# Optimization experiments

Measured on AMD Instinct MI355X. Metric: run time of the kernel, lower is better.

Reference implementation:

```python
import jax, jax.numpy as jnp
import numpy as np

N, G = 10000, 200          # nodes, graphs
EL, EG = 160000, 500000    # local / global edges
S, V = 256, 64             # scalar / vector hidden dims
NA, NB = 16, 5             # atom types, bond types


def _lin(k, i, o):
    return (jax.random.normal(k, (i, o), jnp.float32) / np.sqrt(i))


def scatter_mean(vals, idx, num_segments):
    # vals: [N, ...]; idx: [N] int
    sums = jax.ops.segment_sum(vals, idx, num_segments=num_segments)
    cnt = jax.ops.segment_sum(jnp.ones((vals.shape[0],), vals.dtype), idx,
                              num_segments=num_segments)
    cnt = jnp.maximum(cnt, 1.0).reshape((-1,) + (1,) * (vals.ndim - 1))
    return sums / cnt


def calc_edge_attrs(edge_index, pos):
    src, tgt = edge_index[0], edge_index[1]
    r = pos[tgt] - pos[src]                      # [E,3]
    a = (pos[tgt] * pos[src]).sum(-1)            # [E]
    d = jnp.sqrt(jnp.clip((r ** 2).sum(-1), 1e-6))
    r_norm = r / d[:, None]
    return d, a, r_norm


def setup_inputs() -> dict:
    key = jax.random.key(0)
    ks = jax.random.split(key, 24)
    inp = {}
    inp["x"] = jax.random.normal(ks[0], (N, NA), jnp.float32)
    inp["t"] = jax.random.uniform(ks[1], (G, 1), jnp.float32)
    inp["pos"] = jax.random.normal(ks[2], (N, 3), jnp.float32)
    eil = jax.random.randint(ks[3], (2, EL), 0, N)
    eig = jax.random.randint(ks[4], (2, EG), 0, N)
    # avoid self-edges so edge distances are strictly positive (safe sqrt grads)
    eig = eig.at[1].set(jnp.where(eig[1] == eig[0], (eig[1] + 1) % N, eig[1]))
    eil = eil.at[1].set(jnp.where(eil[1] == eil[0], (eil[1] + 1) % N, eil[1]))
    inp["edge_index_local"] = eil
    inp["edge_index_global"] = eig
    inp["edge_attr_global"] = jax.random.normal(ks[5], (EG, NB), jnp.float32)
    inp["batch"] = jnp.sort(jax.random.randint(ks[6], (N,), 0, G))
    # learned parameters
    inp["W_time"], inp["b_time"] = _lin(ks[7], 1, S), jnp.zeros((S,), jnp.float32)
    inp["W_atom"], inp["b_atom"] = _lin(ks[8], NA, S), jnp.zeros((S,), jnp.float32)
    inp["W_at"], inp["b_at"] = _lin(ks[9], S, S), jnp.zeros((S,), jnp.float32)
    inp["W_shared"], inp["b_shared"] = _lin(ks[10], S, S), jnp.zeros((S,), jnp.float32)
    inp["W_b0"], inp["b_b0"] = _lin(ks[11], S + 1, S), jnp.zeros((S,), jnp.float32)
    inp["W_b1"], inp["b_b1"] = _lin(ks[12], S, 2 * NB), jnp.zeros((2 * NB,), jnp.float32)
    inp["W_coord"] = _lin(ks[13], V, 2)           # no bias
    inp["W_atoms"], inp["b_atoms"] = _lin(ks[14], S, 2 * NA), jnp.zeros((2 * NA,), jnp.float32)
    return inp


def reference(x, t, pos, edge_attr_global, W_time, b_time, W_atom, b_atom,
              W_at, b_at, W_shared, b_shared, W_b0, b_b0, W_b1, b_b1,
              W_coord, W_atoms, b_atoms,
              edge_index_local, edge_index_global, batch):
    # --- trunk: center positions, embed atoms + time ---
    pos = pos - scatter_mean(pos, batch, G)[batch]
    temb = t @ W_time + b_time                    # [G,S]
    tnode = temb[batch]                           # [N,S]
    s = x @ W_atom + b_atom
    s = (s + tnode) @ W_at + b_at                 # [N,S]
    # --- edge attrs (gather-compute pattern feeding the GNN) ---
    d_l, a_l, rn_l = calc_edge_attrs(edge_index_local, pos)
    d_g, a_g, rn_g = calc_edge_attrs(edge_index_global, pos)
    # GNN stand-in (identity on s, v, p): v initialized to zeros as in original
    v = jnp.zeros((N, 3, V), s.dtype)
    # --- prediction head ---
    s = jax.nn.silu(s @ W_shared + b_shared)
    j, i = edge_index_global[0], edge_index_global[1]
    d = jnp.sqrt(((pos[i] - pos[j]) ** 2).sum(-1, keepdims=True))  # [EG,1]
    edge = jnp.concatenate([s[i] + s[j], d], axis=-1)              # [EG,S+1]
    bonds = jax.nn.silu(edge @ W_b0 + b_b0) @ W_b1 + b_b1          # [EG,2*NB]
    bonds_pred, bonds_eps = bonds[:, :NB], bonds[:, NB:]
    coords = jnp.einsum('nkv,vo->nko', v, W_coord)                 # [N,3,2]
    coords = coords - scatter_mean(coords, batch, G)[batch]
    coords_eps0, coords_eps1 = coords[..., 0], coords[..., 1]      # [N,3]
    atoms = s @ W_atoms + b_atoms                                  # [N,2*NA]
    atoms_eps, atoms_pred = atoms[:, :NA], atoms[:, NA:]
    pos_c = pos - scatter_mean(pos, batch, G)[batch]
    coords_pred = pos_c + coords_eps1
    return (coords_pred, coords_eps0, atoms_pred, atoms_eps,
            bonds_pred, bonds_eps, d_l, rn_l, a_g, rn_g)
```

## Files before the change

kernel.cpp:

```cpp
#include <hip/hip_runtime.h>
#include <hip/hip_bf16.h>

typedef __hip_bfloat16 bf16;
typedef short bf16x8 __attribute__((ext_vector_type(8)));
typedef float f32x4 __attribute__((ext_vector_type(4)));
typedef float f32x2 __attribute__((ext_vector_type(2)));

#define N_NODES  10000
#define G_GRAPHS 200
#define EL_EDGES 160000
#define EG_EDGES 500000
#define S_DIM    256
#define APAD     264

#define WS_FLAG   0
#define WS_POSC   1024
#define WS_WD     31232
#define WS_BB0    31488
#define WS_BB1    34304
#define WS_WATOM  34560
#define WS_WTIME  38656
#define WS_BTIME  38912
#define WS_BATOM  39168
#define WS_BAT    39424
#define WS_BSH    39680
#define WS_BATOMS 39936
#define WS_T      40000
#define WS_X      40448
#define WT_AT     200448
#define WT_SH     233216
#define WT_B0     265984
#define WT_ATOMS  298752
#define WT_B1     302848
#define WS_H      304896
#define WS_END_FLOATS (WS_H + (N_NODES * S_DIM) / 4)

#define CHAN(S)    ((((S) >> 6) << 6) + (((S) & 3) << 4) + (((S) & 63) >> 2))
#define CHANINV(k) ((((k) >> 6) << 6) + (((k) & 15) << 2) + (((k) >> 4) & 3))

#define O_CPRED 0
#define O_CEPS  30000
#define O_APRED 60000
#define O_AEPS  220000
#define O_BPRED 380000
#define O_BEPS  2880000
#define O_DL    5380000
#define O_RNL   5540000
#define O_AG    6020000
#define O_RNG   6520000

__device__ __forceinline__ float b2f(bf16 v) { return __bfloat162float(v); }
__device__ __forceinline__ bf16  f2b(float v) { return __float2bfloat16(v); }
__device__ __forceinline__ unsigned short bbits(float v) {
    bf16 b = f2b(v);
    return *reinterpret_cast<unsigned short*>(&b);
}
__device__ __forceinline__ float ldin(const void* p, int idx, int isf32) {
    return isf32 ? ((const float*)p)[idx] : b2f(((const bf16*)p)[idx]);
}
__device__ __forceinline__ void stout(void* out, int f32o, size_t idx, float v) {
    if (f32o) ((float*)out)[idx] = v;
    else      ((bf16*)out)[idx]  = f2b(v);
}
__device__ __forceinline__ float silu(float p) {
    return p * __builtin_amdgcn_rcpf(1.0f + __expf(-p));
}
__device__ __forceinline__ int dtype_f32(const void* tt) {
    const unsigned short* q = (const unsigned short*)tt;
    int c = 0;
#pragma unroll
    for (int z = 0; z < 32; ++z) c += (q[z] >= 0x4000) ? 1 : 0;
    return c > 0;
}

__global__ void k_prep(const void* __restrict__ x, const void* __restrict__ tt,
                       const void* __restrict__ W_time, const void* __restrict__ b_time,
                       const void* __restrict__ W_atom, const void* __restrict__ b_atom,
                       const void* __restrict__ W_at, const void* __restrict__ b_at,
                       const void* __restrict__ W_shared, const void* __restrict__ b_shared,
                       const void* __restrict__ W_b0, const void* __restrict__ b_b0,
                       const void* __restrict__ W_b1, const void* __restrict__ b_b1,
                       const void* __restrict__ W_atoms, const void* __restrict__ b_atoms,
                       float* __restrict__ ws) {
    const int t = blockIdx.x * blockDim.x + threadIdx.x;
    const int f = dtype_f32(tt);
    if (t == 0) ws[WS_FLAG] = f ? 1.0f : 0.0f;
    if (t < 65536) {
        const int k = t >> 8, n = t & 255;
        ((unsigned short*)(ws + WT_AT))[n * 256 + k] = bbits(ldin(W_at, t, f));
        ((unsigned short*)(ws + WT_SH))[n * 256 + k] = bbits(ldin(W_shared, t, f));
        ((unsigned short*)(ws + WT_B0))[n * 256 + k] = bbits(ldin(W_b0, t, f));
    }
    if (t < 160000) ws[WS_X + t] = ldin(x, t, f);
    if (t < 8192) {
        const int k = t >> 5, n = t & 31;
        ((unsigned short*)(ws + WT_ATOMS))[n * 256 + k] = bbits(ldin(W_atoms, t, f));
    }
    if (t < 4096) ws[WS_WATOM + t] = ldin(W_atom, t, f);
    if (t < 2560) {
        const int k = t / 10, n = t - k * 10;
        ((unsigned short*)(ws + WT_B1))[n * 256 + CHANINV(k)] = bbits(ldin(W_b1, t, f));
    } else if (t < 4096) {
        ((unsigned short*)(ws + WT_B1))[t] = 0;
    }
    if (t < 256) {
        ws[WS_WD + t]    = ldin(W_b0, 65536 + CHAN(t), f);
        ws[WS_BB0 + t]   = ldin(b_b0, CHAN(t), f);
        ws[WS_WTIME + t] = ldin(W_time, t, f);
        ws[WS_BTIME + t] = ldin(b_time, t, f);
        ws[WS_BATOM + t] = ldin(b_atom, t, f);
        ws[WS_BAT + t]   = ldin(b_at, t, f);
        ws[WS_BSH + t]   = ldin(b_shared, t, f);
    }
    if (t < 200) ws[WS_T + t] = ldin(tt, t, f);
    if (t < 32)  ws[WS_BATOMS + t] = ldin(b_atoms, t, f);
    if (t < 16)  ws[WS_BB1 + t] = (t < 10) ? ldin(b_b1, t, f) : 0.0f;
}

__global__ void k_pos(const void* __restrict__ pos, const int* __restrict__ batch,
                      float* __restrict__ ws, void* __restrict__ out) {
    const int g = blockIdx.x;
    const int f32o = ws[WS_FLAG] != 0.0f;
    __shared__ int s_lo, s_hi;
    __shared__ float wsum[4][3];
    __shared__ float mean[3];
    if (threadIdx.x == 0) {
        int lo = 0, hi = N_NODES;
        while (lo < hi) { int m = (lo + hi) >> 1; if (batch[m] < g) lo = m + 1; else hi = m; }
        s_lo = lo;
        int lo2 = lo; hi = N_NODES;
        while (lo2 < hi) { int m = (lo2 + hi) >> 1; if (batch[m] < g + 1) lo2 = m + 1; else hi = m; }
        s_hi = lo2;
    }
    __syncthreads();
    const int lo = s_lo, hi = s_hi, cnt = hi - lo;
    float sx = 0.f, sy = 0.f, sz = 0.f;
    for (int n = lo + threadIdx.x; n < hi; n += 256) {
        sx += ldin(pos, n * 3 + 0, f32o);
        sy += ldin(pos, n * 3 + 1, f32o);
        sz += ldin(pos, n * 3 + 2, f32o);
    }
#pragma unroll
    for (int off = 32; off > 0; off >>= 1) {
        sx += __shfl_down(sx, off);
        sy += __shfl_down(sy, off);
        sz += __shfl_down(sz, off);
    }
    if ((threadIdx.x & 63) == 0) {
        wsum[threadIdx.x >> 6][0] = sx;
        wsum[threadIdx.x >> 6][1] = sy;
        wsum[threadIdx.x >> 6][2] = sz;
    }
    __syncthreads();
    if (threadIdx.x == 0) {
        float inv = 1.0f / (float)max(cnt, 1);
        mean[0] = (wsum[0][0] + wsum[1][0] + wsum[2][0] + wsum[3][0]) * inv;
        mean[1] = (wsum[0][1] + wsum[1][1] + wsum[2][1] + wsum[3][1]) * inv;
        mean[2] = (wsum[0][2] + wsum[1][2] + wsum[2][2] + wsum[3][2]) * inv;
    }
    __syncthreads();
    for (int n = lo + threadIdx.x; n < hi; n += 256) {
#pragma unroll
        for (int k = 0; k < 3; ++k) {
            float p = ldin(pos, n * 3 + k, f32o) - mean[k];
            ws[WS_POSC + n * 3 + k] = p;
            stout(out, f32o, O_CPRED + n * 3 + k, p);
            stout(out, f32o, O_CEPS + n * 3 + k, 0.0f);
        }
    }
}

__global__ __launch_bounds__(256) void k_node(
    const int* __restrict__ batch, const float* __restrict__ ws,
    unsigned int* __restrict__ h_out, void* __restrict__ out) {
    __shared__ unsigned short actA[16][APAD];
    __shared__ unsigned short actB[16][APAD];
    const int tid = threadIdx.x;
    const int wave = tid >> 6, lane = tid & 63;
    const int quad = lane >> 4, l16 = lane & 15;
    const int row0 = blockIdx.x * 16;

    {
        const int r = tid >> 4;
        const int c0 = (tid & 15) * 16;
        const int g = row0 + r;
        float tb = ws[WS_T + batch[g]];
        float xr[16];
#pragma unroll
        for (int k = 0; k < 16; ++k) xr[k] = ws[WS_X + g * 16 + k];
        for (int cc = 0; cc < 16; cc += 4) {
            const int c = c0 + cc;
            float a0 = ws[WS_BATOM + c + 0] + tb * ws[WS_WTIME + c + 0] + ws[WS_BTIME + c + 0];
            float a1 = ws[WS_BATOM + c + 1] + tb * ws[WS_WTIME + c + 1] + ws[WS_BTIME + c + 1];
            float a2 = ws[WS_BATOM + c + 2] + tb * ws[WS_WTIME + c + 2] + ws[WS_BTIME + c + 2];
            float a3 = ws[WS_BATOM + c + 3] + tb * ws[WS_WTIME + c + 3] + ws[WS_BTIME + c + 3];
#pragma unroll
            for (int k = 0; k < 16; ++k) {
                float4 w4 = *(const float4*)(ws + WS_WATOM + k * S_DIM + c);
                a0 += xr[k] * w4.x; a1 += xr[k] * w4.y;
                a2 += xr[k] * w4.z; a3 += xr[k] * w4.w;
            }
            actA[r][c + 0] = bbits(a0); actA[r][c + 1] = bbits(a1);
            actA[r][c + 2] = bbits(a2); actA[r][c + 3] = bbits(a3);
        }
    }
    __syncthreads();

    const unsigned short* wt_at = (const unsigned short*)(ws + WT_AT);
    const unsigned short* wt_sh = (const unsigned short*)(ws + WT_SH);
    const unsigned short* wt_b0 = (const unsigned short*)(ws + WT_B0);
    const unsigned short* wt_am = (const unsigned short*)(ws + WT_ATOMS);
    const int n0 = wave * 64;

    {
        f32x4 acc[4] = {};
        for (int kk = 0; kk < S_DIM; kk += 32) {
            const int k = kk + quad * 8;
            bf16x8 a = *(const bf16x8*)&actA[l16][k];
#pragma unroll
            for (int nt = 0; nt < 4; ++nt) {
                bf16x8 b = *(const bf16x8*)(wt_at + (size_t)(n0 + nt * 16 + l16) * S_DIM + k);
                acc[nt] = __builtin_amdgcn_mfma_f32_16x16x32_bf16(a, b, acc[nt], 0, 0, 0);
            }
        }
#pragma unroll
        for (int nt = 0; nt < 4; ++nt) {
            const int n = n0 + nt * 16 + l16;
            const float bv = ws[WS_BAT + n];
#pragma unroll
            for (int r = 0; r < 4; ++r)
                actB[quad * 4 + r][n] = bbits(acc[nt][r] + bv);
        }
    }
    __syncthreads();

    {
        f32x4 acc[4] = {};
        for (int kk = 0; kk < S_DIM; kk += 32) {
            const int k = kk + quad * 8;
            bf16x8 a = *(const bf16x8*)&actB[l16][k];
#pragma unroll
            for (int nt = 0; nt < 4; ++nt) {
                bf16x8 b = *(const bf16x8*)(wt_sh + (size_t)(n0 + nt * 16 + l16) * S_DIM + k);
                acc[nt] = __builtin_amdgcn_mfma_f32_16x16x32_bf16(a, b, acc[nt], 0, 0, 0);
            }
        }
        __syncthreads();
#pragma unroll
        for (int nt = 0; nt < 4; ++nt) {
            const int n = n0 + nt * 16 + l16;
            const float bv = ws[WS_BSH + n];
#pragma unroll
            for (int r = 0; r < 4; ++r)
                actA[quad * 4 + r][n] = bbits(silu(acc[nt][r] + bv));
        }
    }
    __syncthreads();

    {
        f32x4 acc[4] = {};
        for (int kk = 0; kk < S_DIM; kk += 32) {
            const int k = kk + quad * 8;
            bf16x8 a = *(const bf16x8*)&actA[l16][k];
#pragma unroll
            for (int nt = 0; nt < 4; ++nt) {
                bf16x8 b = *(const bf16x8*)(wt_b0 + (size_t)(n0 + nt * 16 + l16) * S_DIM + k);
                acc[nt] = __builtin_amdgcn_mfma_f32_16x16x32_bf16(a, b, acc[nt], 0, 0, 0);
            }
        }
#pragma unroll
        for (int r = 0; r < 4; ++r) {
            const int g = row0 + quad * 4 + r;
            int w = 0;
            w = __builtin_amdgcn_cvt_pk_fp8_f32(acc[0][r], acc[1][r], w, false);
            w = __builtin_amdgcn_cvt_pk_fp8_f32(acc[2][r], acc[3][r], w, true);
            h_out[(size_t)g * 64 + wave * 16 + l16] = (unsigned int)w;
        }
    }

    if (wave < 2) {
        f32x4 acc = {};
        const int n = wave * 16 + l16;
        for (int kk = 0; kk < S_DIM; kk += 32) {
            const int k = kk + quad * 8;
            bf16x8 a = *(const bf16x8*)&actA[l16][k];
            bf16x8 b = *(const bf16x8*)(wt_am + (size_t)n * S_DIM + k);
            acc = __builtin_amdgcn_mfma_f32_16x16x32_bf16(a, b, acc, 0, 0, 0);
        }
        const float bv = ws[WS_BATOMS + n];
        const int f32o = ws[WS_FLAG] != 0.0f;
#pragma unroll
        for (int r = 0; r < 4; ++r) {
            const int g = row0 + quad * 4 + r;
            float v = acc[r] + bv;
            if (n < 16) stout(out, f32o, O_AEPS + (size_t)g * 16 + n, v);
            else        stout(out, f32o, O_APRED + (size_t)g * 16 + (n - 16), v);
        }
    }
}

__global__ void k_local(const int* __restrict__ ei, const float* __restrict__ ws,
                        void* __restrict__ out) {
    int e = blockIdx.x * blockDim.x + threadIdx.x;
    if (e >= EL_EDGES) return;
    const int f32o = ws[WS_FLAG] != 0.0f;
    const float* posc = ws + WS_POSC;
    int s = ei[e];
    int t = ei[EL_EDGES + e];
    float rx = posc[t * 3 + 0] - posc[s * 3 + 0];
    float ry = posc[t * 3 + 1] - posc[s * 3 + 1];
    float rz = posc[t * 3 + 2] - posc[s * 3 + 2];
    float dsq = rx * rx + ry * ry + rz * rz;
    float d = sqrtf(fmaxf(dsq, 1e-6f));
    float inv = 1.0f / d;
    stout(out, f32o, O_DL + e, d);
    stout(out, f32o, O_RNL + e * 3 + 0, rx * inv);
    stout(out, f32o, O_RNL + e * 3 + 1, ry * inv);
    stout(out, f32o, O_RNL + e * 3 + 2, rz * inv);
}

__global__ __launch_bounds__(256) void k_bonds(const int* __restrict__ ei,
                                               const float* __restrict__ ws,
                                               const unsigned char* __restrict__ h,
                                               void* __restrict__ out) {
    __shared__ unsigned char sm[4][32][272];
    const int wave = threadIdx.x >> 6, lane = threadIdx.x & 63;
    const int quad = lane >> 4, l16 = lane & 15;
    const int e0 = blockIdx.x * 64 + wave * 16;
    const int f32o = ws[WS_FLAG] != 0.0f;

    uint4 tmp[8];
#pragma unroll
    for (int p = 0; p < 8; ++p) {
        const int row = p * 4 + quad;
        const int es = e0 + (row & 15);
        const int ecs = es < EG_EDGES ? es : (EG_EDGES - 1);
        const int node = (row < 16) ? ei[EG_EDGES + ecs] : ei[ecs];
        tmp[p] = *(const uint4*)(h + (size_t)node * 256 + l16 * 16);
    }
#pragma unroll
    for (int p = 0; p < 8; ++p) {
        const int row = p * 4 + quad;
        *(uint4*)&sm[wave][row][l16 * 16] = tmp[p];
    }

    const int e = e0 + l16;
    const bool ev = e < EG_EDGES;
    const int ec = ev ? e : (EG_EDGES - 1);
    const int j = ei[ec];
    const int i = ei[EG_EDGES + ec];
    const float* posc = ws + WS_POSC;
    float pix = posc[i * 3 + 0], piy = posc[i * 3 + 1], piz = posc[i * 3 + 2];
    float pjx = posc[j * 3 + 0], pjy = posc[j * 3 + 1], pjz = posc[j * 3 + 2];
    float rx = pix - pjx, ry = piy - pjy, rz = piz - pjz;
    float dsq = rx * rx + ry * ry + rz * rz;
    float d = sqrtf(dsq);

    if (quad == 0 && ev) {
        float ag = pix * pjx + piy * pjy + piz * pjz;
        float inv = 1.0f / sqrtf(fmaxf(dsq, 1e-6f));
        stout(out, f32o, O_AG + e, ag);
        stout(out, f32o, O_RNG + (size_t)e * 3 + 0, rx * inv);
        stout(out, f32o, O_RNG + (size_t)e * 3 + 1, ry * inv);
        stout(out, f32o, O_RNG + (size_t)e * 3 + 2, rz * inv);
    }

    const float* __restrict__ wd  = ws + WS_WD;
    const float* __restrict__ bb0 = ws + WS_BB0;
    const unsigned short* __restrict__ wb1t = (const unsigned short*)(ws + WT_B1);

    f32x4 acc = {};
#pragma unroll
    for (int t = 0; t < 8; ++t) {
        const int k = t * 32 + quad * 8;
        uint2 uaw = *(const uint2*)&sm[wave][l16][k];
        uint2 ubw = *(const uint2*)&sm[wave][16 + l16][k];
        float4 wA = *(const float4*)(wd + k);
        float4 wB = *(const float4*)(wd + k + 4);
        float4 bA = *(const float4*)(bb0 + k);
        float4 bB = *(const float4*)(bb0 + k + 4);
        f32x2 a01 = __builtin_amdgcn_cvt_pk_f32_fp8((int)uaw.x, false);
        f32x2 a23 = __builtin_amdgcn_cvt_pk_f32_fp8((int)uaw.x, true);
        f32x2 a45 = __builtin_amdgcn_cvt_pk_f32_fp8((int)uaw.y, false);
        f32x2 a67 = __builtin_amdgcn_cvt_pk_f32_fp8((int)uaw.y, true);
        f32x2 b01 = __builtin_amdgcn_cvt_pk_f32_fp8((int)ubw.x, false);
        f32x2 b23 = __builtin_amdgcn_cvt_pk_f32_fp8((int)ubw.x, true);
        f32x2 b45 = __builtin_amdgcn_cvt_pk_f32_fp8((int)ubw.y, false);
        f32x2 b67 = __builtin_amdgcn_cvt_pk_f32_fp8((int)ubw.y, true);
        union { bf16x8 v; unsigned short s[8]; } af;
        af.s[0] = bbits(silu(a01.x + b01.x + fmaf(d, wA.x, bA.x)));
        af.s[1] = bbits(silu(a01.y + b01.y + fmaf(d, wA.y, bA.y)));
        af.s[2] = bbits(silu(a23.x + b23.x + fmaf(d, wA.z, bA.z)));
        af.s[3] = bbits(silu(a23.y + b23.y + fmaf(d, wA.w, bA.w)));
        af.s[4] = bbits(silu(a45.x + b45.x + fmaf(d, wB.x, bB.x)));
        af.s[5] = bbits(silu(a45.y + b45.y + fmaf(d, wB.y, bB.y)));
        af.s[6] = bbits(silu(a67.x + b67.x + fmaf(d, wB.z, bB.z)));
        af.s[7] = bbits(silu(a67.y + b67.y + fmaf(d, wB.w, bB.w)));
        bf16x8 bfr = *(const bf16x8*)(wb1t + (size_t)l16 * S_DIM + k);
        acc = __builtin_amdgcn_mfma_f32_16x16x32_bf16(af.v, bfr, acc, 0, 0, 0);
    }

    if (l16 < 10) {
        const float bv = ws[WS_BB1 + l16];
#pragma unroll
        for (int r = 0; r < 4; ++r) {
            const int er = e0 + quad * 4 + r;
            if (er < EG_EDGES) {
                float v = acc[r] + bv;
                if (l16 < 5) stout(out, f32o, O_BPRED + (size_t)er * 5 + l16, v);
                else         stout(out, f32o, O_BEPS + (size_t)er * 5 + (l16 - 5), v);
            }
        }
    }
}

extern "C" void kernel_launch(void* const* d_in, const int* in_sizes, int n_in,
                              void* d_out, int out_size, void* d_ws, size_t ws_size,
                              hipStream_t stream) {
    const void* x        = d_in[0];
    const void* t        = d_in[1];
    const void* pos      = d_in[2];
    const int*  eil      = (const int*)d_in[3];
    const int*  eig      = (const int*)d_in[4];
    const int*  batch    = (const int*)d_in[6];
    const void* W_time   = d_in[7];
    const void* b_time   = d_in[8];
    const void* W_atom   = d_in[9];
    const void* b_atom   = d_in[10];
    const void* W_at     = d_in[11];
    const void* b_at     = d_in[12];
    const void* W_shared = d_in[13];
    const void* b_shared = d_in[14];
    const void* W_b0     = d_in[15];
    const void* b_b0     = d_in[16];
    const void* W_b1     = d_in[17];
    const void* b_b1     = d_in[18];
    const void* W_atoms  = d_in[20];
    const void* b_atoms  = d_in[21];
    (void)in_sizes; (void)n_in; (void)out_size;

    const size_t NEED = (size_t)WS_END_FLOATS * sizeof(float);
    if (ws_size < NEED) return;

    float* ws = (float*)d_ws;
    unsigned int* hbuf = (unsigned int*)(ws + WS_H);

    k_prep<<<640, 256, 0, stream>>>(x, t, W_time, b_time, W_atom, b_atom,
                                    W_at, b_at, W_shared, b_shared, W_b0, b_b0,
                                    W_b1, b_b1, W_atoms, b_atoms, ws);
    k_pos<<<G_GRAPHS, 256, 0, stream>>>(pos, batch, ws, d_out);
    k_node<<<N_NODES / 16, 256, 0, stream>>>(batch, ws, hbuf, d_out);
    k_local<<<(EL_EDGES + 255) / 256, 256, 0, stream>>>(eil, ws, d_out);
    k_bonds<<<(EG_EDGES + 63) / 64, 256, 0, stream>>>(eig, ws,
                                                      (const unsigned char*)hbuf, d_out);
}
```

Baseline: 250.7 us.

## Merge local-edge and bond kernels; split bond K-dimension across wave pairs

Fuses the local-edge geometry kernel into the bond kernel as extra trailing blocks, removing one launch and its tail. Each 16-edge tile is now handled by two waves that each gather one endpoint's features and compute half of the K=256 reduction, combining partial MFMA accumulators through shared memory. This doubles the number of waves per edge, which raises parallelism for the gather-heavy workload, at the cost of added block-wide barriers and a shared-memory reduction step. Bounds checks are dropped because the edge counts divide the tile sizes exactly.

```diff
diff --git a/kernel.cpp b/kernel.cpp
--- a/kernel.cpp
+++ b/kernel.cpp
@@ -12,6 +12,9 @@
 #define EG_EDGES 500000
 #define S_DIM    256
 #define APAD     264
+
+#define BONDS_BLOCKS 15625
+#define LOCAL_BLOCKS 625
 
 #define WS_FLAG   0
 #define WS_POSC   1024
@@ -299,82 +302,84 @@
     }
 }
 
-__global__ void k_local(const int* __restrict__ ei, const float* __restrict__ ws,
-                        void* __restrict__ out) {
-    int e = blockIdx.x * blockDim.x + threadIdx.x;
-    if (e >= EL_EDGES) return;
+__global__ __launch_bounds__(256, 6) void k_edges(const int* __restrict__ eig,
+                                                  const int* __restrict__ eil,
+                                                  const float* __restrict__ ws,
+                                                  const unsigned char* __restrict__ h,
+                                                  void* __restrict__ out) {
+    __shared__ unsigned char sm[2][32][272];
     const int f32o = ws[WS_FLAG] != 0.0f;
-    const float* posc = ws + WS_POSC;
-    int s = ei[e];
-    int t = ei[EL_EDGES + e];
-    float rx = posc[t * 3 + 0] - posc[s * 3 + 0];
-    float ry = posc[t * 3 + 1] - posc[s * 3 + 1];
-    float rz = posc[t * 3 + 2] - posc[s * 3 + 2];
-    float dsq = rx * rx + ry * ry + rz * rz;
-    float d = sqrtf(fmaxf(dsq, 1e-6f));
-    float inv = 1.0f / d;
-    stout(out, f32o, O_DL + e, d);
-    stout(out, f32o, O_RNL + e * 3 + 0, rx * inv);
-    stout(out, f32o, O_RNL + e * 3 + 1, ry * inv);
-    stout(out, f32o, O_RNL + e * 3 + 2, rz * inv);
-}
-
-__global__ __launch_bounds__(256) void k_bonds(const int* __restrict__ ei,
-                                               const float* __restrict__ ws,
-                                               const unsigned char* __restrict__ h,
-                                               void* __restrict__ out) {
-    __shared__ unsigned char sm[4][32][272];
+
+    if (blockIdx.x >= BONDS_BLOCKS) {
+        const int e = (blockIdx.x - BONDS_BLOCKS) * 256 + threadIdx.x;
+        const float* posc = ws + WS_POSC;
+        const int s = eil[e];
+        const int t = eil[EL_EDGES + e];
+        float rx = posc[t * 3 + 0] - posc[s * 3 + 0];
+        float ry = posc[t * 3 + 1] - posc[s * 3 + 1];
+        float rz = posc[t * 3 + 2] - posc[s * 3 + 2];
+        float dsq = rx * rx + ry * ry + rz * rz;
+        float d = sqrtf(fmaxf(dsq, 1e-6f));
+        float inv = 1.0f / d;
+        stout(out, f32o, O_DL + e, d);
+        stout(out, f32o, O_RNL + (size_t)e * 3 + 0, rx * inv);
+        stout(out, f32o, O_RNL + (size_t)e * 3 + 1, ry * inv);
+        stout(out, f32o, O_RNL + (size_t)e * 3 + 2, rz * inv);
+        return;
+    }
+
     const int wave = threadIdx.x >> 6, lane = threadIdx.x & 63;
     const int quad = lane >> 4, l16 = lane & 15;
-    const int e0 = blockIdx.x * 64 + wave * 16;
-    const int f32o = ws[WS_FLAG] != 0.0f;
-
-    uint4 tmp[8];
-#pragma unroll
-    for (int p = 0; p < 8; ++p) {
-        const int row = p * 4 + quad;
-        const int es = e0 + (row & 15);
-        const int ecs = es < EG_EDGES ? es : (EG_EDGES - 1);
-        const int node = (row < 16) ? ei[EG_EDGES + ecs] : ei[ecs];
+    const int P = wave >> 1, sub = wave & 1;
+    const int e0 = blockIdx.x * 32 + P * 16;
+
+    uint4 tmp[4];
+#pragma unroll
+    for (int p = 0; p < 4; ++p) {
+        const int r16 = p * 4 + quad;
+        const int es = e0 + r16;
+        const int node = sub ? eig[es] : eig[EG_EDGES + es];
         tmp[p] = *(const uint4*)(h + (size_t)node * 256 + l16 * 16);
     }
 #pragma unroll
-    for (int p = 0; p < 8; ++p) {
-        const int row = p * 4 + quad;
-        *(uint4*)&sm[wave][row][l16 * 16] = tmp[p];
-    }
-
-    const int e = e0 + l16;
-    const bool ev = e < EG_EDGES;
-    const int ec = ev ? e : (EG_EDGES - 1);
-    const int j = ei[ec];
-    const int i = ei[EG_EDGES + ec];
-    const float* posc = ws + WS_POSC;
-    float pix = posc[i * 3 + 0], piy = posc[i * 3 + 1], piz = posc[i * 3 + 2];
-    float pjx = posc[j * 3 + 0], pjy = posc[j * 3 + 1], pjz = posc[j * 3 + 2];
-    float rx = pix - pjx, ry = piy - pjy, rz = piz - pjz;
-    float dsq = rx * rx + ry * ry + rz * rz;
-    float d = sqrtf(dsq);
-
-    if (quad == 0 && ev) {
-        float ag = pix * pjx + piy * pjy + piz * pjz;
-        float inv = 1.0f / sqrtf(fmaxf(dsq, 1e-6f));
-        stout(out, f32o, O_AG + e, ag);
-        stout(out, f32o, O_RNG + (size_t)e * 3 + 0, rx * inv);
-        stout(out, f32o, O_RNG + (size_t)e * 3 + 1, ry * inv);
-        stout(out, f32o, O_RNG + (size_t)e * 3 + 2, rz * inv);
-    }
-
+    for (int p = 0; p < 4; ++p) {
+        const int row = sub * 16 + p * 4 + quad;
+        *(uint4*)&sm[P][row][l16 * 16] = tmp[p];
+    }
+
+    if (sub == 0) {
+        const int e = e0 + l16;
+        const int j = eig[e];
+        const int i = eig[EG_EDGES + e];
+        const float* posc = ws + WS_POSC;
+        float pix = posc[i * 3 + 0], piy = posc[i * 3 + 1], piz = posc[i * 3 + 2];
+        float pjx = posc[j * 3 + 0], pjy = posc[j * 3 + 1], pjz = posc[j * 3 + 2];
+        float rx = pix - pjx, ry = piy - pjy, rz = piz - pjz;
+        float dsq = rx * rx + ry * ry + rz * rz;
+        if (quad == 0) {
+            float ag = pix * pjx + piy * pjy + piz * pjz;
+            float inv = 1.0f / sqrtf(fmaxf(dsq, 1e-6f));
+            stout(out, f32o, O_AG + e, ag);
+            stout(out, f32o, O_RNG + (size_t)e * 3 + 0, rx * inv);
+            stout(out, f32o, O_RNG + (size_t)e * 3 + 1, ry * inv);
+            stout(out, f32o, O_RNG + (size_t)e * 3 + 2, rz * inv);
+            *(float*)&sm[P][l16][256] = sqrtf(dsq);
+        }
+    }
+    __syncthreads();
+
+    const float d = *(const float*)&sm[P][l16][256];
     const float* __restrict__ wd  = ws + WS_WD;
     const float* __restrict__ bb0 = ws + WS_BB0;
     const unsigned short* __restrict__ wb1t = (const unsigned short*)(ws + WT_B1);
 
+    const int kbase = sub * 128;
     f32x4 acc = {};
 #pragma unroll
-    for (int t = 0; t < 8; ++t) {
-        const int k = t * 32 + quad * 8;
-        uint2 uaw = *(const uint2*)&sm[wave][l16][k];
-        uint2 ubw = *(const uint2*)&sm[wave][16 + l16][k];
+    for (int t = 0; t < 4; ++t) {
+        const int k = kbase + t * 32 + quad * 8;
+        uint2 uaw = *(const uint2*)&sm[P][l16][k];
+        uint2 ubw = *(const uint2*)&sm[P][16 + l16][k];
         float4 wA = *(const float4*)(wd + k);
         float4 wB = *(const float4*)(wd + k + 4);
         float4 bA = *(const float4*)(bb0 + k);
@@ -400,16 +405,19 @@
         acc = __builtin_amdgcn_mfma_f32_16x16x32_bf16(af.v, bfr, acc, 0, 0, 0);
     }
 
-    if (l16 < 10) {
+    __syncthreads();
+    f32x4* sc = (f32x4*)&sm[P][0][0];
+    if (sub == 1) sc[lane] = acc;
+    __syncthreads();
+    if (sub == 0 && l16 < 10) {
+        f32x4 o = sc[lane];
         const float bv = ws[WS_BB1 + l16];
 #pragma unroll
         for (int r = 0; r < 4; ++r) {
             const int er = e0 + quad * 4 + r;
-            if (er < EG_EDGES) {
-                float v = acc[r] + bv;
-                if (l16 < 5) stout(out, f32o, O_BPRED + (size_t)er * 5 + l16, v);
-                else         stout(out, f32o, O_BEPS + (size_t)er * 5 + (l16 - 5), v);
-            }
+            float v = acc[r] + o[r] + bv;
+            if (l16 < 5) stout(out, f32o, O_BPRED + (size_t)er * 5 + l16, v);
+            else         stout(out, f32o, O_BEPS + (size_t)er * 5 + (l16 - 5), v);
         }
     }
 }
@@ -450,7 +458,6 @@
                                     W_b1, b_b1, W_atoms, b_atoms, ws);
     k_pos<<<G_GRAPHS, 256, 0, stream>>>(pos, batch, ws, d_out);
     k_node<<<N_NODES / 16, 256, 0, stream>>>(batch, ws, hbuf, d_out);
-    k_local<<<(EL_EDGES + 255) / 256, 256, 0, stream>>>(eil, ws, d_out);
-    k_bonds<<<(EG_EDGES + 63) / 64, 256, 0, stream>>>(eig, ws,
-                                                      (const unsigned char*)hbuf, d_out);
-}
+    k_edges<<<BONDS_BLOCKS + LOCAL_BLOCKS, 256, 0, stream>>>(
+        eig, eil, ws, (const unsigned char*)hbuf, d_out);
+}
```

Measured after the change: 251.0 us. Within noise of the previous version (+0.1%).
